# Performance work log

Hardware: AMD Instinct MI355X
Metric: run time of the kernel (lower is better)

The kernel has to match this reference:

```python
import jax, jax.numpy as jnp
import numpy as np

# dims: B batch, N spectrum bins, C top-k peaks, K sparse_k, H heads, DH head dim,
# DM hidden, DI role/filler dim (outer_product mode), L layers, S memory slots, OUT classes
B, N, C, K, H, DH, DM, DI, L, S, OUT = 2, 2048, 256, 64, 4, 32, 128, 16, 3, 64, 10


def _gelu(x):
    return jax.nn.gelu(x, approximate=False)  # torch default gelu is exact erf


def _ln(x, g, b, eps=1e-5):
    m = x.mean(-1, keepdims=True)
    v = x.var(-1, keepdims=True)
    return (x - m) / jnp.sqrt(v + eps) * g + b


def setup_inputs() -> dict:
    key = jax.random.key(0)
    ks = iter(jax.random.split(key, 64))
    def p(shape, s=0.05):
        return jax.random.normal(next(ks), shape, jnp.float32) * s
    return {
        "x": jax.random.uniform(next(ks), (B, N), jnp.float32),
        "emb_roles": p((N, DI)),
        "filler_w": p((DI,)),
        "conv_w": p((DI, 1, 5)),
        "conv_b": p((DI,)),
        "outer_w": p((DM, DI * DI)),
        "enc_ng": jnp.ones((DM,), jnp.float32), "enc_nb": jnp.zeros((DM,), jnp.float32),
        "qw": p((L, DM, DM)), "qb": p((L, DM)),
        "kw": p((L, DM, DM)), "kb": p((L, DM)),
        "vw": p((L, DM, DM)), "vb": p((L, DM)),
        "rel_w1": p((L, DH, 3 * DH)), "rel_b1": p((L, DH)),
        "rel_w2": p((L, 1, DH)), "rel_b2": p((L, 1)),
        "ow": p((L, DM, DM)), "ob": p((L, DM)),
        "n1g": jnp.ones((L, DM), jnp.float32), "n1b": jnp.zeros((L, DM), jnp.float32),
        "n2g": jnp.ones((L, DM), jnp.float32), "n2b": jnp.zeros((L, DM), jnp.float32),
        "ffn_w1": p((L, 4 * DM, DM)), "ffn_b1": p((L, 4 * DM)),
        "ffn_w2": p((L, DM, 4 * DM)), "ffn_b2": p((L, DM)),
        "task_query": p((DM,)),
        "slots": p((S, DM)),
        "gru_wih": p((3 * DM, DM)), "gru_whh": p((3 * DM, DM)),
        "gru_bih": p((3 * DM,)), "gru_bhh": p((3 * DM,)),
        "mem_ng": jnp.ones((DM,), jnp.float32), "mem_nb": jnp.zeros((DM,), jnp.float32),
        "head_w": p((OUT, DM)), "head_b": p((OUT,)),
    }


def reference(x, emb_roles, filler_w, conv_w, conv_b, outer_w, enc_ng, enc_nb,
              qw, qb, kw, kb, vw, vb, rel_w1, rel_b1, rel_w2, rel_b2, ow, ob,
              n1g, n1b, n2g, n2b, ffn_w1, ffn_b1, ffn_w2, ffn_b2,
              task_query, slots, gru_wih, gru_whh, gru_bih, gru_bhh,
              mem_ng, mem_nb, head_w, head_b):
    # --- top-k peak selection ---
    x_log = jnp.log1p(jnp.maximum(x, 0.0))
    vals, top_idx = jax.lax.top_k(x_log, C)          # (B,C)
    mz = top_idx.astype(jnp.float32)                  # curr_mz = top_idx.float()
    # --- MultiScaleBindingEncoder ---
    half = DI // 2
    freq = jnp.exp(jnp.arange(half, dtype=jnp.float32) * (-np.log(10000.0) / (half - 1)))
    ang = mz[..., None] * freq                        # (B,C,half)
    roles = jnp.concatenate([jnp.sin(ang), jnp.cos(ang)], -1) + emb_roles[:C][None]  # (B,C,DI)
    f_point = vals[..., None] * filler_w              # Linear(1,DI,no bias)
    xp = jnp.pad(vals, ((0, 0), (2, 2)), mode='reflect')[:, None, :]  # reflection pad k//2
    f_local = jax.lax.conv_general_dilated(xp, conv_w, (1,), 'VALID',
                                           dimension_numbers=('NCW', 'OIW', 'NCW'))
    f_local = _gelu(f_local.transpose(0, 2, 1) + conv_b)
    fillers = _gelu(f_point + f_local)                # (B,C,DI)
    outer = jnp.einsum('bcd,bce->bcde', roles, fillers).reshape(B, C, DI * DI)
    bnd = _ln(outer @ outer_w.T, enc_ng, enc_nb)      # (B,C,DM)
    scale = 1.0 / np.sqrt(DH)
    for i in range(L):
        # --- SparseSecondOrderAttention ---
        q = (bnd @ qw[i].T + qb[i]).reshape(B, C, H, DH).transpose(0, 2, 1, 3)  # (B,H,C,d)
        k = (bnd @ kw[i].T + kb[i]).reshape(B, C, H, DH).transpose(0, 2, 1, 3)
        v = (bnd @ vw[i].T + vb[i]).reshape(B, C, H, DH).transpose(0, 2, 1, 3)
        w1 = rel_w1[i]                                # (d, 3d)
        qp = q @ w1[:, :DH].T
        kp = k @ w1[:, DH:2 * DH].T
        res = qp[:, :, :, None, :] + kp[:, :, None, :, :] + rel_b1[i]           # (B,H,C,C,d)
        res = res + (q[:, :, :, None, :] * k[:, :, None, :, :]) @ w1[:, 2 * DH:].T
        scores = (_gelu(res) @ rel_w2[i].T + rel_b2[i])[..., 0] * scale         # (B,H,C,C)
        minv = jax.lax.top_k(scores, K)[0][..., -1:]  # kth largest per row
        scores = jnp.where(scores >= minv, scores, jnp.float32(-1e9))
        attn = jax.nn.softmax(scores, -1)             # dropout is identity in eval
        out = (attn @ v).transpose(0, 2, 1, 3).reshape(B, C, DM)
        b1 = _ln(bnd + out @ ow[i].T + ob[i], n1g[i], n1b[i])
        ff = _gelu(b1 @ ffn_w1[i].T + ffn_b1[i]) @ ffn_w2[i].T + ffn_b2[i]
        bnd = _ln(b1 + ff, n2g[i], n2b[i])
    # --- TaskQueryReadoutPlus ---
    dms = 1.0 / np.sqrt(DM)
    sc = jnp.einsum('d,bcd->bc', task_query, bnd) * dms
    h = jnp.einsum('bc,bcd->bd', jax.nn.softmax(sc, -1), bnd)
    # --- GatedRelationalMemory ---
    sl = jnp.broadcast_to(slots[None], (B, S, DM))
    sc2 = jnp.einsum('bsd,bcd->bsc', sl, bnd) * dms
    ctx = jnp.einsum('bsc,bcd->bsd', jax.nn.softmax(sc2, -1), bnd)
    gi = ctx @ gru_wih.T + gru_bih
    gh = sl @ gru_whh.T + gru_bhh
    ir, iz, inn = jnp.split(gi, 3, -1)
    hr, hz, hn = jnp.split(gh, 3, -1)
    r = jax.nn.sigmoid(ir + hr)
    z = jax.nn.sigmoid(iz + hz)
    n = jnp.tanh(inn + r * hn)
    mem = _ln(((1.0 - z) * n + z * sl).mean(1), mem_ng, mem_nb)
    return (h + mem) @ head_w.T + head_b
```

## Files before the change

kernel.cpp:

```cpp
#include <hip/hip_runtime.h>
#include <hip/hip_bf16.h>
#include <math.h>

#define Bb 2
#define Nn 2048
#define Cc 256
#define Kk 64
#define Hh 4
#define DHh 32
#define DMm 128
#define DIi 16
#define Ll 3
#define Ss 64
#define OUTn 10

__device__ __forceinline__ float gelu_exact(float x) {
    return 0.5f * x * (1.0f + erff(x * 0.70710678118654752f));
}

__device__ __forceinline__ float dot128_4(const float* a, const float* __restrict__ w) {
    float s0 = 0.f, s1 = 0.f, s2 = 0.f, s3 = 0.f;
#pragma unroll
    for (int e = 0; e < 128; e += 4) {
        s0 = fmaf(a[e],     w[e],     s0);
        s1 = fmaf(a[e + 1], w[e + 1], s1);
        s2 = fmaf(a[e + 2], w[e + 2], s2);
        s3 = fmaf(a[e + 3], w[e + 3], s3);
    }
    return (s0 + s1) + (s2 + s3);
}

__global__ __launch_bounds__(1024) void k_topk(const float* __restrict__ x,
                                               float* __restrict__ vals,
                                               float* __restrict__ mz) {
    __shared__ float key[Nn];
    __shared__ int   idx[Nn];
    const int b = blockIdx.x, t = threadIdx.x;
    for (int i = t; i < Nn; i += 1024) { key[i] = x[b * Nn + i]; idx[i] = i; }
    __syncthreads();
    for (int k = 2; k <= Nn; k <<= 1) {
        for (int j = k >> 1; j > 0; j >>= 1) {
            for (int i = t; i < Nn; i += 1024) {
                int ixj = i ^ j;
                if (ixj > i) {
                    float va = key[i], vb = key[ixj];
                    int ia = idx[i], ib = idx[ixj];
                    bool aG = (va > vb) || (va == vb && ia < ib);
                    bool desc = ((i & k) == 0);
                    bool dosw = desc ? (!aG) : aG;
                    if (dosw) { key[i] = vb; key[ixj] = va; idx[i] = ib; idx[ixj] = ia; }
                }
            }
            __syncthreads();
        }
    }
    if (t < Cc) {
        vals[b * Cc + t] = log1pf(fmaxf(key[t], 0.f));
        mz[b * Cc + t] = (float)idx[t];
    }
}

__global__ __launch_bounds__(256) void k_encode(const float* __restrict__ vals,
                                                const float* __restrict__ mz,
                                                const float* __restrict__ emb_roles,
                                                const float* __restrict__ filler_w,
                                                const float* __restrict__ conv_w,
                                                const float* __restrict__ conv_b,
                                                const float* __restrict__ outer_w,
                                                const float* __restrict__ g,
                                                const float* __restrict__ bb,
                                                float* __restrict__ bnd) {
    __shared__ float roles[DIi], fill[DIi], outerv[256], ps[2][128];
    __shared__ float redA[4], redB[4];
    const int bc = blockIdx.x;
    const int b = bc >> 8, c = bc & 255;
    const int t = threadIdx.x;
    const float NEG = -1.3157629102823120f;
    if (t < DIi) {
        float mzv = mz[bc];
        float rr;
        if (t < 8) rr = sinf(mzv * expf((float)t * NEG));
        else       rr = cosf(mzv * expf((float)(t - 8) * NEG));
        roles[t] = rr + emb_roles[c * DIi + t];
    } else if (t < 2 * DIi) {
        int e = t - DIi;
        float vc = vals[bc];
        float fp = vc * filler_w[e];
        float acc = conv_b[e];
#pragma unroll
        for (int kk = 0; kk < 5; ++kk) {
            int pos = c - 2 + kk;
            pos = pos < 0 ? -pos : (pos >= Cc ? 2 * Cc - 2 - pos : pos);
            acc = fmaf(vals[b * Cc + pos], conv_w[e * 5 + kk], acc);
        }
        fill[e] = gelu_exact(fp + gelu_exact(acc));
    }
    __syncthreads();
    outerv[t] = roles[t >> 4] * fill[t & 15];
    __syncthreads();
    const int o = t & 127, seg = t >> 7;
    float acc = dot128_4(outerv + seg * 128, outer_w + o * 256 + seg * 128);
    ps[seg][o] = acc;
    __syncthreads();
    float t1 = 0.f;
    if (t < 128) t1 = ps[0][t] + ps[1][t];
    float sa = (t < 128) ? t1 : 0.f, sb = (t < 128) ? t1 * t1 : 0.f;
#pragma unroll
    for (int off = 1; off < 64; off <<= 1) { sa += __shfl_xor(sa, off); sb += __shfl_xor(sb, off); }
    if ((t & 63) == 0) { redA[t >> 6] = sa; redB[t >> 6] = sb; }
    __syncthreads();
    float S = (redA[0] + redA[1]) + (redA[2] + redA[3]);
    float Q = (redB[0] + redB[1]) + (redB[2] + redB[3]);
    float mean = S * (1.f / 128.f);
    float var = Q * (1.f / 128.f) - mean * mean;
    if (t < 128) bnd[bc * DMm + t] = (t1 - mean) / sqrtf(var + 1e-5f) * g[t] + bb[t];
}

__global__ __launch_bounds__(128) void k_qkv(const float* __restrict__ bnd,
                                             const float* __restrict__ qw, const float* __restrict__ qb,
                                             const float* __restrict__ kw, const float* __restrict__ kb,
                                             const float* __restrict__ vw, const float* __restrict__ vb,
                                             const float* __restrict__ w1,
                                             float* __restrict__ q, float* __restrict__ k,
                                             float* __restrict__ v, float* __restrict__ qp,
                                             float* __restrict__ kp) {
    __shared__ float brow[DMm], prow[DMm];
    const int bid = blockIdx.x;
    const int which = bid >> 9;
    const int bc = bid & 511;
    const int b = bc >> 8, c = bc & 255;
    const int t = threadIdx.x;
    brow[t] = bnd[bc * DMm + t];
    __syncthreads();
    const float* w  = (which == 0) ? qw : (which == 1) ? kw : vw;
    const float* bi = (which == 0) ? qb : (which == 1) ? kb : vb;
    float val = bi[t] + dot128_4(brow, w + t * DMm);
    const int h = t >> 5, d = t & 31;
    const int gi = ((b * Hh + h) * Cc + c) * DHh + d;
    float* outp = (which == 0) ? q : (which == 1) ? k : v;
    outp[gi] = val;
    if (which < 2) {
        prow[t] = val;
        __syncthreads();
        const float* wr = w1 + d * 96 + ((which == 1) ? 32 : 0);
        float acc = 0.f;
#pragma unroll
        for (int e = 0; e < DHh; ++e) acc = fmaf(prow[h * 32 + e], wr[e], acc);
        ((which == 0) ? qp : kp)[gi] = acc;
    }
}

__global__ __launch_bounds__(256) void k_attn(const float* __restrict__ q,
                                              const float* __restrict__ k,
                                              const float* __restrict__ v,
                                              const float* __restrict__ qp,
                                              const float* __restrict__ kp,
                                              const float* __restrict__ w1,
                                              const float* __restrict__ rb1,
                                              const float* __restrict__ w2,
                                              const float* __restrict__ rb2,
                                              float* __restrict__ aout) {
    __shared__ float w3s[DHh * DHh];
    __shared__ float qs[DHh], qps[DHh], rb1s[DHh], w2s[DHh];
    __shared__ float scL[Cc], aw[Cc], pr[Cc];
    const int bid = blockIdx.x;
    const int t = threadIdx.x;
    const int lane = t & 63;
    const int i = bid & 255, bh = bid >> 8;
    const int rowbase = (bh * Cc + i) * DHh;

    {
        int row = t >> 3, c4 = t & 7;
        float4 vv = *reinterpret_cast<const float4*>(w1 + row * 96 + 64 + c4 * 4);
        *reinterpret_cast<float4*>(&w3s[row * 32 + c4 * 4]) = vv;
    }
    if (t < 32) {
        qs[t]   = q[rowbase + t];
        qps[t]  = qp[rowbase + t];
        rb1s[t] = rb1[t];
        w2s[t]  = w2[t];
    }
    __syncthreads();
    const float rb2v = rb2[0];

    float score;
    {
        const int jb = (bh * Cc + t) * DHh;
        float kr[32], kpr[32];
        const float4* k4  = reinterpret_cast<const float4*>(k + jb);
        const float4* kp4 = reinterpret_cast<const float4*>(kp + jb);
#pragma unroll
        for (int m = 0; m < 8; ++m) {
            float4 a = k4[m];  kr[4*m] = a.x; kr[4*m+1] = a.y; kr[4*m+2] = a.z; kr[4*m+3] = a.w;
            float4 bq = kp4[m]; kpr[4*m] = bq.x; kpr[4*m+1] = bq.y; kpr[4*m+2] = bq.z; kpr[4*m+3] = bq.w;
        }
        float p[32];
#pragma unroll
        for (int e = 0; e < 32; ++e) p[e] = qs[e] * kr[e];
        float acc = 0.f;
#pragma unroll 4
        for (int d = 0; d < 32; ++d) {
            const float* wr = &w3s[d * 32];
            float r0 = qps[d] + rb1s[d] + kpr[d], r1 = 0.f, r2 = 0.f, r3 = 0.f;
#pragma unroll
            for (int e = 0; e < 8; ++e) {
                r0 = fmaf(p[e],      wr[e],      r0);
                r1 = fmaf(p[8 + e],  wr[8 + e],  r1);
                r2 = fmaf(p[16 + e], wr[16 + e], r2);
                r3 = fmaf(p[24 + e], wr[24 + e], r3);
            }
            float rr = (r0 + r1) + (r2 + r3);
            acc = fmaf(gelu_exact(rr), w2s[d], acc);
        }
        score = (acc + rb2v) * 0.17677669529663689f;
    }
    scL[t] = score;
    __syncthreads();

    float v0 = scL[lane], v1 = scL[64 + lane], v2 = scL[128 + lane], v3 = scL[192 + lane];
    auto cx_lane = [&](int k_, int j_) {
        float o0 = __shfl_xor(v0, j_), o1 = __shfl_xor(v1, j_);
        float o2 = __shfl_xor(v2, j_), o3 = __shfl_xor(v3, j_);
        bool lower = ((lane & j_) == 0);
        bool d0 = (((0 * 64 + lane) & k_) == 0);
        bool d1 = (((1 * 64 + lane) & k_) == 0);
        bool d2 = (((2 * 64 + lane) & k_) == 0);
        bool d3 = (((3 * 64 + lane) & k_) == 0);
        v0 = (lower == d0) ? fmaxf(v0, o0) : fminf(v0, o0);
        v1 = (lower == d1) ? fmaxf(v1, o1) : fminf(v1, o1);
        v2 = (lower == d2) ? fmaxf(v2, o2) : fminf(v2, o2);
        v3 = (lower == d3) ? fmaxf(v3, o3) : fminf(v3, o3);
    };
    auto cx_reg1 = [&](int k_) {
        bool dA = (((0 * 64) & k_) == 0);
        bool dB = (((2 * 64) & k_) == 0);
        float aA = v0, bA = v1;
        v0 = dA ? fmaxf(aA, bA) : fminf(aA, bA);
        v1 = dA ? fminf(aA, bA) : fmaxf(aA, bA);
        float aB = v2, bB = v3;
        v2 = dB ? fmaxf(aB, bB) : fminf(aB, bB);
        v3 = dB ? fminf(aB, bB) : fmaxf(aB, bB);
    };
    auto cx_reg2 = [&](int k_) {
        bool dA = (((0 * 64) & k_) == 0);
        bool dB = (((1 * 64) & k_) == 0);
        float aA = v0, bA = v2;
        v0 = dA ? fmaxf(aA, bA) : fminf(aA, bA);
        v2 = dA ? fminf(aA, bA) : fmaxf(aA, bA);
        float aB = v1, bB = v3;
        v1 = dB ? fmaxf(aB, bB) : fminf(aB, bB);
        v3 = dB ? fminf(aB, bB) : fmaxf(aB, bB);
    };
    cx_lane(2, 1);
    cx_lane(4, 2); cx_lane(4, 1);
    cx_lane(8, 4); cx_lane(8, 2); cx_lane(8, 1);
    cx_lane(16, 8); cx_lane(16, 4); cx_lane(16, 2); cx_lane(16, 1);
    cx_lane(32, 16); cx_lane(32, 8); cx_lane(32, 4); cx_lane(32, 2); cx_lane(32, 1);
    cx_lane(64, 32); cx_lane(64, 16); cx_lane(64, 8); cx_lane(64, 4); cx_lane(64, 2); cx_lane(64, 1);
    cx_reg1(128);
    cx_lane(128, 32); cx_lane(128, 16); cx_lane(128, 8); cx_lane(128, 4); cx_lane(128, 2); cx_lane(128, 1);
    cx_reg2(256); cx_reg1(256);
    cx_lane(256, 32); cx_lane(256, 16); cx_lane(256, 8); cx_lane(256, 4); cx_lane(256, 2); cx_lane(256, 1);

    const float minv = __shfl(v0, 63);
    const float mx   = __shfl(v0, 0);

    float ls = 0.f;
    ls += expf(v0 - mx);
    ls += (v1 >= minv) ? expf(v1 - mx) : 0.f;
    ls += (v2 >= minv) ? expf(v2 - mx) : 0.f;
    ls += (v3 >= minv) ? expf(v3 - mx) : 0.f;
#pragma unroll
    for (int off = 1; off < 64; off <<= 1) ls += __shfl_xor(ls, off);
    const float inv = 1.f / ls;

    aw[t] = (score >= minv) ? expf(score - mx) * inv : 0.f;
    __syncthreads();

    const int d = t & 31, grp = t >> 5;
    const float* vbp = v + (bh * Cc + grp * 32) * DHh + d;
    const float* awg = aw + grp * 32;
    float a0 = 0.f, a1 = 0.f, a2v = 0.f, a3v = 0.f;
#pragma unroll
    for (int jj = 0; jj < 32; jj += 4) {
        a0  = fmaf(awg[jj],     vbp[jj * 32],       a0);
        a1  = fmaf(awg[jj + 1], vbp[(jj + 1) * 32], a1);
        a2v = fmaf(awg[jj + 2], vbp[(jj + 2) * 32], a2v);
        a3v = fmaf(awg[jj + 3], vbp[(jj + 3) * 32], a3v);
    }
    pr[t] = (a0 + a1) + (a2v + a3v);
    __syncthreads();
    if (t < 32) {
        float o = pr[t];
#pragma unroll
        for (int g2 = 1; g2 < 8; ++g2) o += pr[g2 * 32 + t];
        const int b = bh >> 2, h = bh & 3;
        aout[(b * Cc + i) * DMm + h * DHh + t] = o;
    }
}

__global__ __launch_bounds__(512) void k_ffn(const float* __restrict__ aout,
                                             const float* __restrict__ ow, const float* __restrict__ ob,
                                             const float* __restrict__ n1g, const float* __restrict__ n1b,
                                             const float* __restrict__ fw1, const float* __restrict__ fb1,
                                             const float* __restrict__ fw2, const float* __restrict__ fb2,
                                             const float* __restrict__ n2g, const float* __restrict__ n2b,
                                             float* __restrict__ bnd) {
    __shared__ float arow[DMm], b1row[DMm], ff1[512], ps[4][128];
    __shared__ float redA[8], redB[8], redC[8], redD[8];
    const int bc = blockIdx.x, t = threadIdx.x;
    if (t < 128) arow[t] = aout[bc * DMm + t];
    __syncthreads();
    const int o = t & 127, seg = t >> 7;
    {
        const float* wr = ow + o * DMm + seg * 32;
        const float* ar = arow + seg * 32;
        float pa = 0.f;
#pragma unroll
        for (int e = 0; e < 32; ++e) pa = fmaf(ar[e], wr[e], pa);
        ps[seg][o] = pa;
    }
    __syncthreads();
    float t1 = 0.f;
    if (t < 128) t1 = bnd[bc * DMm + t] + ob[t] + ((ps[0][t] + ps[1][t]) + (ps[2][t] + ps[3][t]));
    float sa = (t < 128) ? t1 : 0.f, sb = (t < 128) ? t1 * t1 : 0.f;
#pragma unroll
    for (int off = 1; off < 64; off <<= 1) { sa += __shfl_xor(sa, off); sb += __shfl_xor(sb, off); }
    if ((t & 63) == 0) { redA[t >> 6] = sa; redB[t >> 6] = sb; }
    __syncthreads();
    float S = 0.f, Q = 0.f;
#pragma unroll
    for (int r = 0; r < 8; ++r) { S += redA[r]; Q += redB[r]; }
    float mean = S * (1.f / 128.f);
    float var = Q * (1.f / 128.f) - mean * mean;
    float b1v = 0.f;
    if (t < 128) {
        b1v = (t1 - mean) / sqrtf(var + 1e-5f) * n1g[t] + n1b[t];
        b1row[t] = b1v;
    }
    __syncthreads();
    ff1[t] = gelu_exact(fb1[t] + dot128_4(b1row, fw1 + t * DMm));
    __syncthreads();
    {
        ps[seg][o] = dot128_4(ff1 + seg * 128, fw2 + o * 512 + seg * 128);
    }
    __syncthreads();
    float t2 = 0.f;
    if (t < 128) t2 = b1v + fb2[t] + ((ps[0][t] + ps[1][t]) + (ps[2][t] + ps[3][t]));
    sa = (t < 128) ? t2 : 0.f; sb = (t < 128) ? t2 * t2 : 0.f;
#pragma unroll
    for (int off = 1; off < 64; off <<= 1) { sa += __shfl_xor(sa, off); sb += __shfl_xor(sb, off); }
    if ((t & 63) == 0) { redC[t >> 6] = sa; redD[t >> 6] = sb; }
    __syncthreads();
    S = 0.f; Q = 0.f;
#pragma unroll
    for (int r = 0; r < 8; ++r) { S += redC[r]; Q += redD[r]; }
    mean = S * (1.f / 128.f);
    var = Q * (1.f / 128.f) - mean * mean;
    if (t < 128) bnd[bc * DMm + t] = (t2 - mean) / sqrtf(var + 1e-5f) * n2g[t] + n2b[t];
}

__global__ __launch_bounds__(256) void k_slots(const float* __restrict__ bnd,
                                               const float* __restrict__ slots,
                                               const float* __restrict__ tq,
                                               const float* __restrict__ wih,
                                               const float* __restrict__ whh,
                                               const float* __restrict__ bih,
                                               const float* __restrict__ bhh,
                                               float* __restrict__ contrib,
                                               float* __restrict__ hbuf) {
    __shared__ float sl[DMm], a2[Cc], ctx2[2][128], ctxs[DMm], giS[3 * DMm], ghS[3 * DMm];
    __shared__ float redM[4], redS[4];
    const int bid = blockIdx.x;
    const int b = bid / 65, s = bid % 65;
    const int t = threadIdx.x;
    if (t < DMm) sl[t] = (s < Ss) ? slots[s * DMm + t] : tq[t];
    __syncthreads();
    float sv = dot128_4(sl, bnd + (b * Cc + t) * DMm) * 0.08838834764831845f;
    float m = sv;
#pragma unroll
    for (int off = 1; off < 64; off <<= 1) m = fmaxf(m, __shfl_xor(m, off));
    if ((t & 63) == 0) redM[t >> 6] = m;
    __syncthreads();
    float mxv = fmaxf(fmaxf(redM[0], redM[1]), fmaxf(redM[2], redM[3]));
    float ev = expf(sv - mxv);
    float su = ev;
#pragma unroll
    for (int off = 1; off < 64; off <<= 1) su += __shfl_xor(su, off);
    if ((t & 63) == 0) redS[t >> 6] = su;
    __syncthreads();
    float sum = (redS[0] + redS[1]) + (redS[2] + redS[3]);
    a2[t] = ev / sum;
    __syncthreads();
    {
        const int o = t & 127, seg = t >> 7;
        float cacc = 0.f;
        for (int cc = 0; cc < 128; ++cc) {
            int c = seg * 128 + cc;
            cacc = fmaf(a2[c], bnd[(b * Cc + c) * DMm + o], cacc);
        }
        ctx2[seg][o] = cacc;
    }
    __syncthreads();
    if (t < DMm) ctxs[t] = ctx2[0][t] + ctx2[1][t];
    __syncthreads();
    if (s == Ss) {
        if (t < DMm) hbuf[b * DMm + t] = ctxs[t];
        return;
    }
    giS[t] = bih[t] + dot128_4(ctxs, wih + t * DMm);
    ghS[t] = bhh[t] + dot128_4(sl, whh + t * DMm);
    if (t < DMm) {
        int o = 256 + t;
        giS[o] = bih[o] + dot128_4(ctxs, wih + o * DMm);
        ghS[o] = bhh[o] + dot128_4(sl, whh + o * DMm);
    }
    __syncthreads();
    if (t < DMm) {
        float r = 1.f / (1.f + expf(-(giS[t] + ghS[t])));
        float z = 1.f / (1.f + expf(-(giS[128 + t] + ghS[128 + t])));
        float n = tanhf(giS[256 + t] + r * ghS[256 + t]);
        contrib[(b * Ss + s) * DMm + t] = (1.f - z) * n + z * sl[t];
    }
}

__global__ __launch_bounds__(128) void k_final(const float* __restrict__ contrib,
                                               const float* __restrict__ hbuf,
                                               const float* __restrict__ mg, const float* __restrict__ mb,
                                               const float* __restrict__ hw, const float* __restrict__ hb,
                                               float* __restrict__ out) {
    __shared__ float hm[DMm], redA[2], redB[2];
    const int b = blockIdx.x, t = threadIdx.x;
    float acc = 0.f;
    for (int s = 0; s < Ss; ++s) acc += contrib[(b * Ss + s) * DMm + t];
    acc *= (1.f / (float)Ss);
    float sa = acc, sb = acc * acc;
#pragma unroll
    for (int off = 1; off < 64; off <<= 1) { sa += __shfl_xor(sa, off); sb += __shfl_xor(sb, off); }
    if ((t & 63) == 0) { redA[t >> 6] = sa; redB[t >> 6] = sb; }
    __syncthreads();
    float S = redA[0] + redA[1], Q = redB[0] + redB[1];
    float mean = S * (1.f / 128.f);
    float var = Q * (1.f / 128.f) - mean * mean;
    float memv = (acc - mean) / sqrtf(var + 1e-5f) * mg[t] + mb[t];
    hm[t] = hbuf[b * DMm + t] + memv;
    __syncthreads();
    if (t < OUTn) {
        float o = hb[t];
        const float* wr = hw + t * DMm;
#pragma unroll 16
        for (int e = 0; e < DMm; ++e) o = fmaf(hm[e], wr[e], o);
        out[b * OUTn + t] = o;
    }
}

extern "C" void kernel_launch(void* const* d_in, const int* in_sizes, int n_in,
                              void* d_out, int out_size, void* d_ws, size_t ws_size,
                              hipStream_t stream) {
    const float* x         = (const float*)d_in[0];
    const float* emb_roles = (const float*)d_in[1];
    const float* filler_w  = (const float*)d_in[2];
    const float* conv_w    = (const float*)d_in[3];
    const float* conv_b    = (const float*)d_in[4];
    const float* outer_w   = (const float*)d_in[5];
    const float* enc_ng    = (const float*)d_in[6];
    const float* enc_nb    = (const float*)d_in[7];
    const float* qw        = (const float*)d_in[8];
    const float* qb        = (const float*)d_in[9];
    const float* kw        = (const float*)d_in[10];
    const float* kb        = (const float*)d_in[11];
    const float* vw        = (const float*)d_in[12];
    const float* vb        = (const float*)d_in[13];
    const float* rel_w1    = (const float*)d_in[14];
    const float* rel_b1    = (const float*)d_in[15];
    const float* rel_w2    = (const float*)d_in[16];
    const float* rel_b2    = (const float*)d_in[17];
    const float* ow        = (const float*)d_in[18];
    const float* ob        = (const float*)d_in[19];
    const float* n1g       = (const float*)d_in[20];
    const float* n1b       = (const float*)d_in[21];
    const float* n2g       = (const float*)d_in[22];
    const float* n2b       = (const float*)d_in[23];
    const float* ffn_w1    = (const float*)d_in[24];
    const float* ffn_b1    = (const float*)d_in[25];
    const float* ffn_w2    = (const float*)d_in[26];
    const float* ffn_b2    = (const float*)d_in[27];
    const float* task_q    = (const float*)d_in[28];
    const float* slots     = (const float*)d_in[29];
    const float* gru_wih   = (const float*)d_in[30];
    const float* gru_whh   = (const float*)d_in[31];
    const float* gru_bih   = (const float*)d_in[32];
    const float* gru_bhh   = (const float*)d_in[33];
    const float* mem_ng    = (const float*)d_in[34];
    const float* mem_nb    = (const float*)d_in[35];
    const float* head_w    = (const float*)d_in[36];
    const float* head_b    = (const float*)d_in[37];

    float* ws = (float*)d_ws;
    const int BC = Bb * Cc;
    const int BHCD = Bb * Hh * Cc * DHh;
    float* valsb = ws;
    float* mzb   = valsb + BC;
    float* bnd   = mzb + BC;
    float* qB    = bnd + BC * DMm;
    float* kB    = qB + BHCD;
    float* vB    = kB + BHCD;
    float* qpB   = vB + BHCD;
    float* kpB   = qpB + BHCD;
    float* aout  = kpB + BHCD;
    float* hbuf  = aout + BC * DMm;
    float* contrib = hbuf + Bb * DMm;

    k_topk<<<Bb, 1024, 0, stream>>>(x, valsb, mzb);
    k_encode<<<BC, 256, 0, stream>>>(valsb, mzb, emb_roles, filler_w, conv_w, conv_b,
                                     outer_w, enc_ng, enc_nb, bnd);
    for (int l = 0; l < Ll; ++l) {
        k_qkv<<<3 * BC, 128, 0, stream>>>(bnd,
                                          qw + l * DMm * DMm, qb + l * DMm,
                                          kw + l * DMm * DMm, kb + l * DMm,
                                          vw + l * DMm * DMm, vb + l * DMm,
                                          rel_w1 + l * DHh * 3 * DHh,
                                          qB, kB, vB, qpB, kpB);
        k_attn<<<Bb * Hh * Cc, 256, 0, stream>>>(qB, kB, vB, qpB, kpB,
                                                 rel_w1 + l * DHh * 3 * DHh,
                                                 rel_b1 + l * DHh,
                                                 rel_w2 + l * DHh,
                                                 rel_b2 + l,
                                                 aout);
        k_ffn<<<BC, 512, 0, stream>>>(aout,
                                      ow + l * DMm * DMm, ob + l * DMm,
                                      n1g + l * DMm, n1b + l * DMm,
                                      ffn_w1 + l * 4 * DMm * DMm, ffn_b1 + l * 4 * DMm,
                                      ffn_w2 + l * 4 * DMm * DMm, ffn_b2 + l * DMm,
                                      n2g + l * DMm, n2b + l * DMm,
                                      bnd);
    }
    k_slots<<<Bb * (Ss + 1), 256, 0, stream>>>(bnd, slots, task_q, gru_wih, gru_whh,
                                               gru_bih, gru_bhh, contrib, hbuf);
    k_final<<<Bb, 128, 0, stream>>>(contrib, hbuf, mem_ng, mem_nb, head_w, head_b, (float*)d_out);
}
```

Before: 498.2 us.

## Fuse QKV projection into encode and FFN kernels; process two heads per attention block

Removes the standalone QKV kernel: layer 0's projections are computed at the end of the encoder kernel, and each later layer's projections at the end of the previous layer's FFN kernel, reusing the normalized row already in shared memory. This cuts one launch per layer and one global round-trip of the hidden state. The attention kernel now handles two heads per block, interleaving their relation-MLP FMAs over the shared weight tile and using float4 accumulation for the attention-times-V step. In exchange, register pressure in the attention kernel rises and the grid shrinks to half as many blocks.

Result: no change. 500.6 us (+0.5%).

```diff
diff --git a/kernel.cpp b/kernel.cpp
--- a/kernel.cpp
+++ b/kernel.cpp
@@ -60,18 +60,26 @@
     }
 }
 
-__global__ __launch_bounds__(256) void k_encode(const float* __restrict__ vals,
-                                                const float* __restrict__ mz,
-                                                const float* __restrict__ emb_roles,
-                                                const float* __restrict__ filler_w,
-                                                const float* __restrict__ conv_w,
-                                                const float* __restrict__ conv_b,
-                                                const float* __restrict__ outer_w,
-                                                const float* __restrict__ g,
-                                                const float* __restrict__ bb,
-                                                float* __restrict__ bnd) {
+__global__ __launch_bounds__(256) void k_enc_qkv(const float* __restrict__ vals,
+                                                 const float* __restrict__ mz,
+                                                 const float* __restrict__ emb_roles,
+                                                 const float* __restrict__ filler_w,
+                                                 const float* __restrict__ conv_w,
+                                                 const float* __restrict__ conv_b,
+                                                 const float* __restrict__ outer_w,
+                                                 const float* __restrict__ g,
+                                                 const float* __restrict__ bb,
+                                                 float* __restrict__ bnd,
+                                                 const float* __restrict__ qw, const float* __restrict__ qb,
+                                                 const float* __restrict__ kw, const float* __restrict__ kb,
+                                                 const float* __restrict__ vw, const float* __restrict__ vb,
+                                                 const float* __restrict__ w1,
+                                                 float* __restrict__ q, float* __restrict__ k,
+                                                 float* __restrict__ v, float* __restrict__ qp,
+                                                 float* __restrict__ kp) {
     __shared__ float roles[DIi], fill[DIi], outerv[256], ps[2][128];
     __shared__ float redA[4], redB[4];
+    __shared__ float bndrow[DMm], qrow[DMm], krow[DMm];
     const int bc = blockIdx.x;
     const int b = bc >> 8, c = bc & 255;
     const int t = threadIdx.x;
@@ -113,40 +121,37 @@
     float Q = (redB[0] + redB[1]) + (redB[2] + redB[3]);
     float mean = S * (1.f / 128.f);
     float var = Q * (1.f / 128.f) - mean * mean;
-    if (t < 128) bnd[bc * DMm + t] = (t1 - mean) / sqrtf(var + 1e-5f) * g[t] + bb[t];
-}
-
-__global__ __launch_bounds__(128) void k_qkv(const float* __restrict__ bnd,
-                                             const float* __restrict__ qw, const float* __restrict__ qb,
-                                             const float* __restrict__ kw, const float* __restrict__ kb,
-                                             const float* __restrict__ vw, const float* __restrict__ vb,
-                                             const float* __restrict__ w1,
-                                             float* __restrict__ q, float* __restrict__ k,
-                                             float* __restrict__ v, float* __restrict__ qp,
-                                             float* __restrict__ kp) {
-    __shared__ float brow[DMm], prow[DMm];
-    const int bid = blockIdx.x;
-    const int which = bid >> 9;
-    const int bc = bid & 511;
-    const int b = bc >> 8, c = bc & 255;
-    const int t = threadIdx.x;
-    brow[t] = bnd[bc * DMm + t];
-    __syncthreads();
-    const float* w  = (which == 0) ? qw : (which == 1) ? kw : vw;
-    const float* bi = (which == 0) ? qb : (which == 1) ? kb : vb;
-    float val = bi[t] + dot128_4(brow, w + t * DMm);
-    const int h = t >> 5, d = t & 31;
-    const int gi = ((b * Hh + h) * Cc + c) * DHh + d;
-    float* outp = (which == 0) ? q : (which == 1) ? k : v;
-    outp[gi] = val;
-    if (which < 2) {
-        prow[t] = val;
-        __syncthreads();
-        const float* wr = w1 + d * 96 + ((which == 1) ? 32 : 0);
-        float acc = 0.f;
-#pragma unroll
-        for (int e = 0; e < DHh; ++e) acc = fmaf(prow[h * 32 + e], wr[e], acc);
-        ((which == 0) ? qp : kp)[gi] = acc;
+    if (t < 128) {
+        float nv = (t1 - mean) / sqrtf(var + 1e-5f) * g[t] + bb[t];
+        bnd[bc * DMm + t] = nv;
+        bndrow[t] = nv;
+    }
+    __syncthreads();
+    {
+        const float* W  = (t < 128) ? qw : kw;
+        const float* Bi = (t < 128) ? qb : kb;
+        float val = Bi[o] + dot128_4(bndrow, W + o * DMm);
+        const int h = o >> 5, dd = o & 31;
+        const int gi = ((b * Hh + h) * Cc + c) * DHh + dd;
+        if (t < 128) { q[gi] = val; qrow[o] = val; }
+        else         { k[gi] = val; krow[o] = val; }
+    }
+    __syncthreads();
+    if (t < 128) {
+        float val = vb[t] + dot128_4(bndrow, vw + t * DMm);
+        const int h = t >> 5, dd = t & 31;
+        v[((b * Hh + h) * Cc + c) * DHh + dd] = val;
+    } else {
+        const int tt = t - 128, h = tt >> 5, dd = tt & 31;
+        const float* wrq = w1 + dd * 96;
+        float aq = 0.f, ak = 0.f;
+#pragma unroll
+        for (int e = 0; e < DHh; ++e) {
+            aq = fmaf(qrow[h * 32 + e], wrq[e],      aq);
+            ak = fmaf(krow[h * 32 + e], wrq[32 + e], ak);
+        }
+        const int gi = ((b * Hh + h) * Cc + c) * DHh + dd;
+        qp[gi] = aq; kp[gi] = ak;
     }
 }
 
@@ -161,13 +166,15 @@
                                               const float* __restrict__ rb2,
                                               float* __restrict__ aout) {
     __shared__ float w3s[DHh * DHh];
-    __shared__ float qs[DHh], qps[DHh], rb1s[DHh], w2s[DHh];
-    __shared__ float scL[Cc], aw[Cc], pr[Cc];
+    __shared__ float qs[2][DHh], qbase[2][DHh], w2s[DHh];
+    __shared__ float scL[2][Cc], aw[2][Cc];
+    __shared__ float4 pr4[2][8][16];
     const int bid = blockIdx.x;
     const int t = threadIdx.x;
-    const int lane = t & 63;
-    const int i = bid & 255, bh = bid >> 8;
-    const int rowbase = (bh * Cc + i) * DHh;
+    const int lane = t & 63, wave = t >> 6;
+    const int i = bid & 255, hp = (bid >> 8) & 1, b = bid >> 9;
+    const int bh0 = (b * Hh + 2 * hp), bh1 = bh0 + 1;
+    const int rb0 = (bh0 * Cc + i) * DHh, rb1o = (bh1 * Cc + i) * DHh;
 
     {
         int row = t >> 3, c4 = t & 7;
@@ -175,140 +182,189 @@
         *reinterpret_cast<float4*>(&w3s[row * 32 + c4 * 4]) = vv;
     }
     if (t < 32) {
-        qs[t]   = q[rowbase + t];
-        qps[t]  = qp[rowbase + t];
-        rb1s[t] = rb1[t];
-        w2s[t]  = w2[t];
+        qs[0][t] = q[rb0 + t];
+        qs[1][t] = q[rb1o + t];
+        float rb = rb1[t];
+        qbase[0][t] = qp[rb0 + t] + rb;
+        qbase[1][t] = qp[rb1o + t] + rb;
+        w2s[t] = w2[t];
     }
     __syncthreads();
     const float rb2v = rb2[0];
 
-    float score;
+    float p0[32], p1[32], base0[32], base1[32];
     {
-        const int jb = (bh * Cc + t) * DHh;
-        float kr[32], kpr[32];
-        const float4* k4  = reinterpret_cast<const float4*>(k + jb);
-        const float4* kp4 = reinterpret_cast<const float4*>(kp + jb);
+        const int jb0 = (bh0 * Cc + t) * DHh;
+        const float4* k4  = reinterpret_cast<const float4*>(k + jb0);
+        const float4* kp4 = reinterpret_cast<const float4*>(kp + jb0);
 #pragma unroll
         for (int m = 0; m < 8; ++m) {
-            float4 a = k4[m];  kr[4*m] = a.x; kr[4*m+1] = a.y; kr[4*m+2] = a.z; kr[4*m+3] = a.w;
-            float4 bq = kp4[m]; kpr[4*m] = bq.x; kpr[4*m+1] = bq.y; kpr[4*m+2] = bq.z; kpr[4*m+3] = bq.w;
-        }
-        float p[32];
-#pragma unroll
-        for (int e = 0; e < 32; ++e) p[e] = qs[e] * kr[e];
-        float acc = 0.f;
+            float4 a = k4[m];
+            p0[4*m]   = qs[0][4*m]   * a.x;
+            p0[4*m+1] = qs[0][4*m+1] * a.y;
+            p0[4*m+2] = qs[0][4*m+2] * a.z;
+            p0[4*m+3] = qs[0][4*m+3] * a.w;
+            float4 bq = kp4[m];
+            base0[4*m]   = qbase[0][4*m]   + bq.x;
+            base0[4*m+1] = qbase[0][4*m+1] + bq.y;
+            base0[4*m+2] = qbase[0][4*m+2] + bq.z;
+            base0[4*m+3] = qbase[0][4*m+3] + bq.w;
+        }
+        const int jb1 = (bh1 * Cc + t) * DHh;
+        const float4* k4b  = reinterpret_cast<const float4*>(k + jb1);
+        const float4* kp4b = reinterpret_cast<const float4*>(kp + jb1);
+#pragma unroll
+        for (int m = 0; m < 8; ++m) {
+            float4 a = k4b[m];
+            p1[4*m]   = qs[1][4*m]   * a.x;
+            p1[4*m+1] = qs[1][4*m+1] * a.y;
+            p1[4*m+2] = qs[1][4*m+2] * a.z;
+            p1[4*m+3] = qs[1][4*m+3] * a.w;
+            float4 bq = kp4b[m];
+            base1[4*m]   = qbase[1][4*m]   + bq.x;
+            base1[4*m+1] = qbase[1][4*m+1] + bq.y;
+            base1[4*m+2] = qbase[1][4*m+2] + bq.z;
+            base1[4*m+3] = qbase[1][4*m+3] + bq.w;
+        }
+    }
+    float acc0 = 0.f, acc1 = 0.f;
 #pragma unroll 4
-        for (int d = 0; d < 32; ++d) {
-            const float* wr = &w3s[d * 32];
-            float r0 = qps[d] + rb1s[d] + kpr[d], r1 = 0.f, r2 = 0.f, r3 = 0.f;
-#pragma unroll
-            for (int e = 0; e < 8; ++e) {
-                r0 = fmaf(p[e],      wr[e],      r0);
-                r1 = fmaf(p[8 + e],  wr[8 + e],  r1);
-                r2 = fmaf(p[16 + e], wr[16 + e], r2);
-                r3 = fmaf(p[24 + e], wr[24 + e], r3);
-            }
-            float rr = (r0 + r1) + (r2 + r3);
-            acc = fmaf(gelu_exact(rr), w2s[d], acc);
-        }
-        score = (acc + rb2v) * 0.17677669529663689f;
-    }
-    scL[t] = score;
-    __syncthreads();
-
-    float v0 = scL[lane], v1 = scL[64 + lane], v2 = scL[128 + lane], v3 = scL[192 + lane];
-    auto cx_lane = [&](int k_, int j_) {
-        float o0 = __shfl_xor(v0, j_), o1 = __shfl_xor(v1, j_);
-        float o2 = __shfl_xor(v2, j_), o3 = __shfl_xor(v3, j_);
-        bool lower = ((lane & j_) == 0);
-        bool d0 = (((0 * 64 + lane) & k_) == 0);
-        bool d1 = (((1 * 64 + lane) & k_) == 0);
-        bool d2 = (((2 * 64 + lane) & k_) == 0);
-        bool d3 = (((3 * 64 + lane) & k_) == 0);
-        v0 = (lower == d0) ? fmaxf(v0, o0) : fminf(v0, o0);
-        v1 = (lower == d1) ? fmaxf(v1, o1) : fminf(v1, o1);
-        v2 = (lower == d2) ? fmaxf(v2, o2) : fminf(v2, o2);
-        v3 = (lower == d3) ? fmaxf(v3, o3) : fminf(v3, o3);
-    };
-    auto cx_reg1 = [&](int k_) {
-        bool dA = (((0 * 64) & k_) == 0);
-        bool dB = (((2 * 64) & k_) == 0);
-        float aA = v0, bA = v1;
-        v0 = dA ? fmaxf(aA, bA) : fminf(aA, bA);
-        v1 = dA ? fminf(aA, bA) : fmaxf(aA, bA);
-        float aB = v2, bB = v3;
-        v2 = dB ? fmaxf(aB, bB) : fminf(aB, bB);
-        v3 = dB ? fminf(aB, bB) : fmaxf(aB, bB);
-    };
-    auto cx_reg2 = [&](int k_) {
-        bool dA = (((0 * 64) & k_) == 0);
-        bool dB = (((1 * 64) & k_) == 0);
-        float aA = v0, bA = v2;
-        v0 = dA ? fmaxf(aA, bA) : fminf(aA, bA);
-        v2 = dA ? fminf(aA, bA) : fmaxf(aA, bA);
-        float aB = v1, bB = v3;
-        v1 = dB ? fmaxf(aB, bB) : fminf(aB, bB);
-        v3 = dB ? fminf(aB, bB) : fmaxf(aB, bB);
-    };
-    cx_lane(2, 1);
-    cx_lane(4, 2); cx_lane(4, 1);
-    cx_lane(8, 4); cx_lane(8, 2); cx_lane(8, 1);
-    cx_lane(16, 8); cx_lane(16, 4); cx_lane(16, 2); cx_lane(16, 1);
-    cx_lane(32, 16); cx_lane(32, 8); cx_lane(32, 4); cx_lane(32, 2); cx_lane(32, 1);
-    cx_lane(64, 32); cx_lane(64, 16); cx_lane(64, 8); cx_lane(64, 4); cx_lane(64, 2); cx_lane(64, 1);
-    cx_reg1(128);
-    cx_lane(128, 32); cx_lane(128, 16); cx_lane(128, 8); cx_lane(128, 4); cx_lane(128, 2); cx_lane(128, 1);
-    cx_reg2(256); cx_reg1(256);
-    cx_lane(256, 32); cx_lane(256, 16); cx_lane(256, 8); cx_lane(256, 4); cx_lane(256, 2); cx_lane(256, 1);
-
-    const float minv = __shfl(v0, 63);
-    const float mx   = __shfl(v0, 0);
-
-    float ls = 0.f;
-    ls += expf(v0 - mx);
-    ls += (v1 >= minv) ? expf(v1 - mx) : 0.f;
-    ls += (v2 >= minv) ? expf(v2 - mx) : 0.f;
-    ls += (v3 >= minv) ? expf(v3 - mx) : 0.f;
-#pragma unroll
-    for (int off = 1; off < 64; off <<= 1) ls += __shfl_xor(ls, off);
-    const float inv = 1.f / ls;
-
-    aw[t] = (score >= minv) ? expf(score - mx) * inv : 0.f;
-    __syncthreads();
-
-    const int d = t & 31, grp = t >> 5;
-    const float* vbp = v + (bh * Cc + grp * 32) * DHh + d;
-    const float* awg = aw + grp * 32;
-    float a0 = 0.f, a1 = 0.f, a2v = 0.f, a3v = 0.f;
-#pragma unroll
-    for (int jj = 0; jj < 32; jj += 4) {
-        a0  = fmaf(awg[jj],     vbp[jj * 32],       a0);
-        a1  = fmaf(awg[jj + 1], vbp[(jj + 1) * 32], a1);
-        a2v = fmaf(awg[jj + 2], vbp[(jj + 2) * 32], a2v);
-        a3v = fmaf(awg[jj + 3], vbp[(jj + 3) * 32], a3v);
-    }
-    pr[t] = (a0 + a1) + (a2v + a3v);
-    __syncthreads();
-    if (t < 32) {
-        float o = pr[t];
-#pragma unroll
-        for (int g2 = 1; g2 < 8; ++g2) o += pr[g2 * 32 + t];
-        const int b = bh >> 2, h = bh & 3;
-        aout[(b * Cc + i) * DMm + h * DHh + t] = o;
-    }
-}
-
-__global__ __launch_bounds__(512) void k_ffn(const float* __restrict__ aout,
-                                             const float* __restrict__ ow, const float* __restrict__ ob,
-                                             const float* __restrict__ n1g, const float* __restrict__ n1b,
-                                             const float* __restrict__ fw1, const float* __restrict__ fb1,
-                                             const float* __restrict__ fw2, const float* __restrict__ fb2,
-                                             const float* __restrict__ n2g, const float* __restrict__ n2b,
-                                             float* __restrict__ bnd) {
+    for (int d = 0; d < 32; ++d) {
+        const float4* w4 = reinterpret_cast<const float4*>(&w3s[d * 32]);
+        float r0 = base0[d], r1 = base1[d];
+#pragma unroll
+        for (int m = 0; m < 8; ++m) {
+            float4 w = w4[m];
+            r0 = fmaf(p0[4*m],   w.x, r0); r1 = fmaf(p1[4*m],   w.x, r1);
+            r0 = fmaf(p0[4*m+1], w.y, r0); r1 = fmaf(p1[4*m+1], w.y, r1);
+            r0 = fmaf(p0[4*m+2], w.z, r0); r1 = fmaf(p1[4*m+2], w.z, r1);
+            r0 = fmaf(p0[4*m+3], w.w, r0); r1 = fmaf(p1[4*m+3], w.w, r1);
+        }
+        float wv = w2s[d];
+        acc0 = fmaf(gelu_exact(r0), wv, acc0);
+        acc1 = fmaf(gelu_exact(r1), wv, acc1);
+    }
+    scL[0][t] = (acc0 + rb2v) * 0.17677669529663689f;
+    scL[1][t] = (acc1 + rb2v) * 0.17677669529663689f;
+    __syncthreads();
+
+    if (wave < 2) {
+        const float* sl = scL[wave];
+        float v0 = sl[lane], v1 = sl[64 + lane], v2 = sl[128 + lane], v3 = sl[192 + lane];
+        auto cx_lane = [&](int k_, int j_) {
+            float o0 = __shfl_xor(v0, j_), o1 = __shfl_xor(v1, j_);
+            float o2 = __shfl_xor(v2, j_), o3 = __shfl_xor(v3, j_);
+            bool lower = ((lane & j_) == 0);
+            bool d0 = (((0 * 64 + lane) & k_) == 0);
+            bool d1 = (((1 * 64 + lane) & k_) == 0);
+            bool d2 = (((2 * 64 + lane) & k_) == 0);
+            bool d3 = (((3 * 64 + lane) & k_) == 0);
+            v0 = (lower == d0) ? fmaxf(v0, o0) : fminf(v0, o0);
+            v1 = (lower == d1) ? fmaxf(v1, o1) : fminf(v1, o1);
+            v2 = (lower == d2) ? fmaxf(v2, o2) : fminf(v2, o2);
+            v3 = (lower == d3) ? fmaxf(v3, o3) : fminf(v3, o3);
+        };
+        auto cx_reg1 = [&](int k_) {
+            bool dA = (((0 * 64) & k_) == 0);
+            bool dB = (((2 * 64) & k_) == 0);
+            float aA = v0, bA = v1;
+            v0 = dA ? fmaxf(aA, bA) : fminf(aA, bA);
+            v1 = dA ? fminf(aA, bA) : fmaxf(aA, bA);
+            float aB = v2, bB = v3;
+            v2 = dB ? fmaxf(aB, bB) : fminf(aB, bB);
+            v3 = dB ? fminf(aB, bB) : fmaxf(aB, bB);
+        };
+        auto cx_reg2 = [&](int k_) {
+            bool dA = (((0 * 64) & k_) == 0);
+            bool dB = (((1 * 64) & k_) == 0);
+            float aA = v0, bA = v2;
+            v0 = dA ? fmaxf(aA, bA) : fminf(aA, bA);
+            v2 = dA ? fminf(aA, bA) : fmaxf(aA, bA);
+            float aB = v1, bB = v3;
+            v1 = dB ? fmaxf(aB, bB) : fminf(aB, bB);
+            v3 = dB ? fminf(aB, bB) : fmaxf(aB, bB);
+        };
+        cx_lane(2, 1);
+        cx_lane(4, 2); cx_lane(4, 1);
+        cx_lane(8, 4); cx_lane(8, 2); cx_lane(8, 1);
+        cx_lane(16, 8); cx_lane(16, 4); cx_lane(16, 2); cx_lane(16, 1);
+        cx_lane(32, 16); cx_lane(32, 8); cx_lane(32, 4); cx_lane(32, 2); cx_lane(32, 1);
+        cx_lane(64, 32); cx_lane(64, 16); cx_lane(64, 8); cx_lane(64, 4); cx_lane(64, 2); cx_lane(64, 1);
+        cx_reg1(128);
+        cx_lane(128, 32); cx_lane(128, 16); cx_lane(128, 8); cx_lane(128, 4); cx_lane(128, 2); cx_lane(128, 1);
+        cx_reg2(256); cx_reg1(256);
+        cx_lane(256, 32); cx_lane(256, 16); cx_lane(256, 8); cx_lane(256, 4); cx_lane(256, 2); cx_lane(256, 1);
+
+        const float minv = __shfl(v0, 63);
+        const float mx   = __shfl(v0, 0);
+        float ls = 0.f;
+        ls += expf(v0 - mx);
+        ls += (v1 >= minv) ? expf(v1 - mx) : 0.f;
+        ls += (v2 >= minv) ? expf(v2 - mx) : 0.f;
+        ls += (v3 >= minv) ? expf(v3 - mx) : 0.f;
+#pragma unroll
+        for (int off = 1; off < 64; off <<= 1) ls += __shfl_xor(ls, off);
+        const float inv = 1.f / ls;
+#pragma unroll
+        for (int r = 0; r < 4; ++r) {
+            int c = r * 64 + lane;
+            float s = sl[c];
+            aw[wave][c] = (s >= minv) ? expf(s - mx) * inv : 0.f;
+        }
+    }
+    __syncthreads();
+
+    {
+        const int h = t >> 7, jg = (t >> 3) & 15, dq = t & 7;
+        const int bh = bh0 + h;
+        const float4* v4 = reinterpret_cast<const float4*>(v) + (size_t)(bh * Cc) * 8 + dq;
+        float4 a4; a4.x = 0.f; a4.y = 0.f; a4.z = 0.f; a4.w = 0.f;
+#pragma unroll
+        for (int jj = 0; jj < 16; ++jj) {
+            int j = jg * 16 + jj;
+            float a = aw[h][j];
+            float4 vv = v4[j * 8];
+            a4.x = fmaf(a, vv.x, a4.x);
+            a4.y = fmaf(a, vv.y, a4.y);
+            a4.z = fmaf(a, vv.z, a4.z);
+            a4.w = fmaf(a, vv.w, a4.w);
+        }
+        pr4[h][dq][jg] = a4;
+    }
+    __syncthreads();
+    if (t < 16) {
+        const int h = t >> 3, dq = t & 7;
+        float4 s; s.x = 0.f; s.y = 0.f; s.z = 0.f; s.w = 0.f;
+#pragma unroll
+        for (int jg = 0; jg < 16; ++jg) {
+            float4 p = pr4[h][dq][jg];
+            s.x += p.x; s.y += p.y; s.z += p.z; s.w += p.w;
+        }
+        float* dst = aout + (b * Cc + i) * DMm + (2 * hp + h) * DHh + dq * 4;
+        *reinterpret_cast<float4*>(dst) = s;
+    }
+}
+
+__global__ __launch_bounds__(512) void k_ffn_qkv(const float* __restrict__ aout,
+                                                 const float* __restrict__ ow, const float* __restrict__ ob,
+                                                 const float* __restrict__ n1g, const float* __restrict__ n1b,
+                                                 const float* __restrict__ fw1, const float* __restrict__ fb1,
+                                                 const float* __restrict__ fw2, const float* __restrict__ fb2,
+                                                 const float* __restrict__ n2g, const float* __restrict__ n2b,
+                                                 float* __restrict__ bnd,
+                                                 int do_qkv,
+                                                 const float* __restrict__ qw, const float* __restrict__ qb,
+                                                 const float* __restrict__ kw, const float* __restrict__ kb,
+                                                 const float* __restrict__ vw, const float* __restrict__ vb,
+                                                 const float* __restrict__ w1,
+                                                 float* __restrict__ q, float* __restrict__ k,
+                                                 float* __restrict__ v, float* __restrict__ qp,
+                                                 float* __restrict__ kp) {
     __shared__ float arow[DMm], b1row[DMm], ff1[512], ps[4][128];
     __shared__ float redA[8], redB[8], redC[8], redD[8];
+    __shared__ float bndrow[DMm], qrow[DMm], krow[DMm];
     const int bc = blockIdx.x, t = threadIdx.x;
+    const int b = bc >> 8, c = bc & 255;
     if (t < 128) arow[t] = aout[bc * DMm + t];
     __syncthreads();
     const int o = t & 127, seg = t >> 7;
@@ -341,9 +397,7 @@
     __syncthreads();
     ff1[t] = gelu_exact(fb1[t] + dot128_4(b1row, fw1 + t * DMm));
     __syncthreads();
-    {
-        ps[seg][o] = dot128_4(ff1 + seg * 128, fw2 + o * 512 + seg * 128);
-    }
+    ps[seg][o] = dot128_4(ff1 + seg * 128, fw2 + o * 512 + seg * 128);
     __syncthreads();
     float t2 = 0.f;
     if (t < 128) t2 = b1v + fb2[t] + ((ps[0][t] + ps[1][t]) + (ps[2][t] + ps[3][t]));
@@ -357,7 +411,37 @@
     for (int r = 0; r < 8; ++r) { S += redC[r]; Q += redD[r]; }
     mean = S * (1.f / 128.f);
     var = Q * (1.f / 128.f) - mean * mean;
-    if (t < 128) bnd[bc * DMm + t] = (t2 - mean) / sqrtf(var + 1e-5f) * n2g[t] + n2b[t];
+    if (t < 128) {
+        float nv = (t2 - mean) / sqrtf(var + 1e-5f) * n2g[t] + n2b[t];
+        bnd[bc * DMm + t] = nv;
+        bndrow[t] = nv;
+    }
+    if (!do_qkv) return;
+    __syncthreads();
+    if (t < 384) {
+        const int which = t >> 7;
+        const float* W  = (which == 0) ? qw : (which == 1) ? kw : vw;
+        const float* Bi = (which == 0) ? qb : (which == 1) ? kb : vb;
+        float val = Bi[o] + dot128_4(bndrow, W + o * DMm);
+        const int h = o >> 5, dd = o & 31;
+        const int gi = ((b * Hh + h) * Cc + c) * DHh + dd;
+        if (which == 0)      { q[gi] = val; qrow[o] = val; }
+        else if (which == 1) { k[gi] = val; krow[o] = val; }
+        else                 { v[gi] = val; }
+    }
+    __syncthreads();
+    if (t < 128) {
+        const int h = t >> 5, dd = t & 31;
+        const float* wrq = w1 + dd * 96;
+        float aq = 0.f, ak = 0.f;
+#pragma unroll
+        for (int e = 0; e < DHh; ++e) {
+            aq = fmaf(qrow[h * 32 + e], wrq[e],      aq);
+            ak = fmaf(krow[h * 32 + e], wrq[32 + e], ak);
+        }
+        const int gi = ((b * Hh + h) * Cc + c) * DHh + dd;
+        qp[gi] = aq; kp[gi] = ak;
+    }
 }
 
 __global__ __launch_bounds__(256) void k_slots(const float* __restrict__ bnd,
@@ -512,28 +596,32 @@
     float* contrib = hbuf + Bb * DMm;
 
     k_topk<<<Bb, 1024, 0, stream>>>(x, valsb, mzb);
-    k_encode<<<BC, 256, 0, stream>>>(valsb, mzb, emb_roles, filler_w, conv_w, conv_b,
-                                     outer_w, enc_ng, enc_nb, bnd);
+    k_enc_qkv<<<BC, 256, 0, stream>>>(valsb, mzb, emb_roles, filler_w, conv_w, conv_b,
+                                      outer_w, enc_ng, enc_nb, bnd,
+                                      qw, qb, kw, kb, vw, vb, rel_w1,
+                                      qB, kB, vB, qpB, kpB);
     for (int l = 0; l < Ll; ++l) {
-        k_qkv<<<3 * BC, 128, 0, stream>>>(bnd,
-                                          qw + l * DMm * DMm, qb + l * DMm,
-                                          kw + l * DMm * DMm, kb + l * DMm,
-                                          vw + l * DMm * DMm, vb + l * DMm,
-                                          rel_w1 + l * DHh * 3 * DHh,
+        k_attn<<<Bb * 2 * Cc, 256, 0, stream>>>(qB, kB, vB, qpB, kpB,
+                                                rel_w1 + l * DHh * 3 * DHh,
+                                                rel_b1 + l * DHh,
+                                                rel_w2 + l * DHh,
+                                                rel_b2 + l,
+                                                aout);
+        int nl = l + 1;
+        int do_qkv = (nl < Ll) ? 1 : 0;
+        int wl = do_qkv ? nl : 0;
+        k_ffn_qkv<<<BC, 512, 0, stream>>>(aout,
+                                          ow + l * DMm * DMm, ob + l * DMm,
+                                          n1g + l * DMm, n1b + l * DMm,
+                                          ffn_w1 + l * 4 * DMm * DMm, ffn_b1 + l * 4 * DMm,
+                                          ffn_w2 + l * 4 * DMm * DMm, ffn_b2 + l * DMm,
+                                          n2g + l * DMm, n2b + l * DMm,
+                                          bnd, do_qkv,
+                                          qw + wl * DMm * DMm, qb + wl * DMm,
+                                          kw + wl * DMm * DMm, kb + wl * DMm,
+                                          vw + wl * DMm * DMm, vb + wl * DMm,
+                                          rel_w1 + wl * DHh * 3 * DHh,
                                           qB, kB, vB, qpB, kpB);
-        k_attn<<<Bb * Hh * Cc, 256, 0, stream>>>(qB, kB, vB, qpB, kpB,
-                                                 rel_w1 + l * DHh * 3 * DHh,
-                                                 rel_b1 + l * DHh,
-                                                 rel_w2 + l * DHh,
-                                                 rel_b2 + l,
-                                                 aout);
-        k_ffn<<<BC, 512, 0, stream>>>(aout,
-                                      ow + l * DMm * DMm, ob + l * DMm,
-                                      n1g + l * DMm, n1b + l * DMm,
-                                      ffn_w1 + l * 4 * DMm * DMm, ffn_b1 + l * 4 * DMm,
-                                      ffn_w2 + l * 4 * DMm * DMm, ffn_b2 + l * DMm,
-                                      n2g + l * DMm, n2b + l * DMm,
-                                      bnd);
     }
     k_slots<<<Bb * (Ss + 1), 256, 0, stream>>>(bnd, slots, task_q, gru_wih, gru_whh,
                                                gru_bih, gru_bhh, contrib, hbuf);
```
